# Optimization experiments

Hardware: AMD Instinct MI355X
Metric: run time of the kernel (lower is better)

## Reference

```python
import jax, jax.numpy as jnp
import numpy as np

D_IN = 128      # input_dim == input_edge_dim == output_dim
H = 512         # hidden_dim
D_OUT = 128
O = 100000      # num objects
T = 200000      # num triples/edges


def setup_inputs() -> dict:
    key = jax.random.key(0)
    ks = jax.random.split(key, 12)
    def kaiming(k, fan_in, fan_out):
        # kaiming_normal_ for Linear: std = sqrt(2 / fan_in)
        return jax.random.normal(k, (fan_in, fan_out), jnp.float32) * np.sqrt(2.0 / fan_in)
    obj_vecs = jax.random.normal(ks[0], (O, D_IN), jnp.float32)
    pred_vecs = jax.random.normal(ks[1], (T, D_IN), jnp.float32)
    edges = jax.random.randint(ks[2], (T, 2), 0, O, jnp.int64 if jax.config.jax_enable_x64 else jnp.int32)
    # net1: [3*D_IN -> H -> 2*H + D_OUT], ReLU after each layer
    W1 = kaiming(ks[3], 3 * D_IN, H); b1 = jnp.zeros((H,), jnp.float32)
    W2 = kaiming(ks[4], H, 2 * H + D_OUT); b2 = jnp.zeros((2 * H + D_OUT,), jnp.float32)
    # net2: [H -> H -> D_OUT], ReLU after each layer
    W3 = kaiming(ks[5], H, H); b3 = jnp.zeros((H,), jnp.float32)
    W4 = kaiming(ks[6], H, D_OUT); b4 = jnp.zeros((D_OUT,), jnp.float32)
    return {"obj_vecs": obj_vecs, "pred_vecs": pred_vecs, "edges": edges,
            "W1": W1, "b1": b1, "W2": W2, "b2": b2,
            "W3": W3, "b3": b3, "W4": W4, "b4": b4}


def reference(obj_vecs, pred_vecs, edges, W1, b1, W2, b2, W3, b3, W4, b4):
    s_idx = edges[:, 0]
    o_idx = edges[:, 1]
    # gather + concat: (T, 3*D_IN)
    cur_t = jnp.concatenate([obj_vecs[s_idx], pred_vecs, obj_vecs[o_idx]], axis=1)
    # net1 MLP (final_nonlinearity=True -> ReLU after both layers)
    h = jax.nn.relu(cur_t @ W1 + b1)                 # (T, H)
    new_t = jax.nn.relu(h @ W2 + b2)                 # (T, 2H + D_OUT)
    new_s = new_t[:, :H]
    new_p = new_t[:, H:H + D_OUT]
    new_o = new_t[:, H + D_OUT:]
    # scatter-add pooling over object slots
    n_obj = obj_vecs.shape[0]
    pooled = jnp.zeros((n_obj, H), dtype=obj_vecs.dtype)
    pooled = pooled.at[s_idx].add(new_s).at[o_idx].add(new_o)
    # avg pooling: divide by per-object triple count (clamped at 1)
    ones = jnp.ones((new_s.shape[0],), dtype=obj_vecs.dtype)
    counts = jnp.zeros((n_obj,), dtype=obj_vecs.dtype).at[s_idx].add(ones).at[o_idx].add(ones)
    pooled = pooled / jnp.maximum(counts, 1.0)[:, None]
    # net2 MLP
    new_obj = jax.nn.relu(jax.nn.relu(pooled @ W3 + b3) @ W4 + b4)  # (O, D_OUT)
    return new_obj, new_p
```

## Files before the change

kernel.cpp:

```cpp
#include <hip/hip_runtime.h>
#include <hip/hip_bf16.h>
#include <stdint.h>

typedef __bf16 bf16_t;
typedef __attribute__((ext_vector_type(8))) __bf16 bf16x8;
typedef __attribute__((ext_vector_type(4))) __bf16 bf16x4;
typedef __attribute__((ext_vector_type(4))) float f32x4;

#define O_N 100000
#define T_N 200000
#define LDN 136
#define SCB 98

__device__ __forceinline__ bf16x8 cvt8(const float* p) {
    f32x4 a = *(const f32x4*)p;
    f32x4 b = *(const f32x4*)(p + 4);
    bf16x8 v;
    v[0] = (bf16_t)a[0]; v[1] = (bf16_t)a[1]; v[2] = (bf16_t)a[2]; v[3] = (bf16_t)a[3];
    v[4] = (bf16_t)b[0]; v[5] = (bf16_t)b[1]; v[6] = (bf16_t)b[2]; v[7] = (bf16_t)b[3];
    return v;
}

__device__ __forceinline__ void gload16(const bf16_t* g, bf16_t* l) {
    auto gp = reinterpret_cast<const __attribute__((address_space(1))) void*>(
        reinterpret_cast<uintptr_t>(g));
    auto lp = reinterpret_cast<__attribute__((address_space(3))) void*>(
        reinterpret_cast<uintptr_t>(l));
    __builtin_amdgcn_global_load_lds(gp, lp, 16, 0, 0);
}

__device__ __forceinline__ void swz_block(int& mbase, int& nbase) {
    const int gx   = gridDim.x;
    const int nwg  = gx * gridDim.y;
    const int orig = blockIdx.y * gx + blockIdx.x;
    const int q = nwg >> 3, r = nwg & 7;
    const int xcd = orig & 7, lo = orig >> 3;
    const int base = (xcd < r) ? xcd * (q + 1) : r * (q + 1) + (xcd - r) * q;
    const int id = base + lo;
    nbase = (id % gx) * 128;
    mbase = (id / gx) * 128;
}

template<int MODE, int N, int K>
__launch_bounds__(256)
__global__ void gemm_k(const bf16_t* __restrict__ A,
                       const bf16_t* __restrict__ AobjB,
                       const float*  __restrict__ ApredF,
                       const int*    __restrict__ edges,
                       const float*  __restrict__ countsIn,
                       const bf16_t* __restrict__ Bt,
                       const float*  __restrict__ bias,
                       bf16_t*       __restrict__ CoutB,
                       float*        __restrict__ CoutF,
                       int M)
{
    __shared__ bf16_t smem[32768];
    __shared__ int sIdxL[128], oIdxL[128];

    const int tid  = threadIdx.x;
    const int lane = tid & 63;
    const int wv   = tid >> 6;
    const int wr   = (wv >> 1) * 64;
    const int wc   = (wv & 1) * 64;
    const int fr   = lane & 15;
    const int rowb = tid >> 3;
    const int colS = ((tid & 7) ^ (rowb & 7)) << 3;
    int mbase, nbase;
    swz_block(mbase, nbase);

    if constexpr (MODE == 1) {
        if (tid < 128) {
            int g = mbase + tid; if (g > M - 1) g = M - 1;
            sIdxL[tid] = edges[2 * g];
            oIdxL[tid] = edges[2 * g + 1];
        }
    }
    __syncthreads();

    f32x4 acc[4][4];
    #pragma unroll
    for (int i = 0; i < 4; i++)
        #pragma unroll
        for (int j = 0; j < 4; j++)
            acc[i][j] = (f32x4){0.f, 0.f, 0.f, 0.f};

    auto stage = [&](int p, int k0) {
        bf16_t* lA = smem + p * 16384;
        bf16_t* lB = lA + 8192;
        if constexpr (MODE == 1) {
            if (k0 < 128 || k0 >= 256) {
                const bool sSeg = (k0 < 128);
                const int  seg0 = sSeg ? k0 : (k0 - 256);
                #pragma unroll
                for (int t = 0; t < 4; ++t) {
                    int row = t * 32 + rowb;
                    int gr  = sSeg ? sIdxL[row] : oIdxL[row];
                    gload16(AobjB + (size_t)gr * 128 + seg0 + colS,
                            &lA[t * 2048 + wv * 512]);
                }
            } else {
                #pragma unroll
                for (int t = 0; t < 4; ++t) {
                    int row  = t * 32 + rowb;
                    int grow = mbase + row; if (grow > M - 1) grow = M - 1;
                    bf16x8 v = cvt8(ApredF + (size_t)grow * 128 + (k0 - 128)
                                    + ((tid & 7) << 3));
                    *(bf16x8*)&lA[t * 2048 + rowb * 64 + colS] = v;
                }
            }
        } else {
            #pragma unroll
            for (int t = 0; t < 4; ++t) {
                int row  = t * 32 + rowb;
                int grow = mbase + row; if (grow > M - 1) grow = M - 1;
                gload16(A + (size_t)grow * K + k0 + colS, &lA[t * 2048 + wv * 512]);
            }
        }
        #pragma unroll
        for (int t = 0; t < 4; ++t) {
            int row = t * 32 + rowb;
            gload16(Bt + (size_t)(nbase + row) * K + k0 + colS,
                    &lB[t * 2048 + wv * 512]);
        }
    };

    const int KT = K / 64;
    stage(0, 0);
    asm volatile("s_waitcnt vmcnt(0) lgkmcnt(0)" ::: "memory");
    __builtin_amdgcn_s_barrier();

    int cur = 0;
    for (int kt = 0; kt < KT; ++kt) {
        if (kt + 1 < KT) stage(cur ^ 1, (kt + 1) * 64);
        const bf16_t* lA = smem + cur * 16384;
        const bf16_t* lB = lA + 8192;
        #pragma unroll
        for (int ks8 = 0; ks8 < 8; ks8 += 4) {
            const int c8 = (ks8 + (lane >> 4)) ^ (lane & 7);
            bf16x8 af[4], bfv[4];
            #pragma unroll
            for (int i = 0; i < 4; i++)
                af[i] = *(const bf16x8*)&lA[(wr + i * 16 + fr) * 64 + (c8 << 3)];
            #pragma unroll
            for (int j = 0; j < 4; j++)
                bfv[j] = *(const bf16x8*)&lB[(wc + j * 16 + fr) * 64 + (c8 << 3)];
            #pragma unroll
            for (int i = 0; i < 4; i++)
                #pragma unroll
                for (int j = 0; j < 4; j++) {
                    if constexpr (MODE == 2)
                        acc[i][j] = __builtin_amdgcn_mfma_f32_16x16x32_bf16(
                            bfv[j], af[i], acc[i][j], 0, 0, 0);
                    else
                        acc[i][j] = __builtin_amdgcn_mfma_f32_16x16x32_bf16(
                            af[i], bfv[j], acc[i][j], 0, 0, 0);
                }
        }
        asm volatile("s_waitcnt vmcnt(0) lgkmcnt(0)" ::: "memory");
        __builtin_amdgcn_s_barrier();
        cur ^= 1;
    }

    if constexpr (MODE == 2) {
        const bool isNewp = (nbase == 512);
        const int  cb     = (nbase < 512) ? nbase : (nbase - 128);
        if (isNewp) {
            #pragma unroll
            for (int j = 0; j < 4; j++) {
                int nl = wc + j * 16 + (lane >> 4) * 4;
                f32x4 bv = *(const f32x4*)&bias[nbase + nl];
                #pragma unroll
                for (int i = 0; i < 4; i++) {
                    int ml   = wr + i * 16 + fr;
                    int grow = mbase + ml;
                    if (grow >= M) continue;
                    float v0 = acc[i][j][0] + bv[0]; v0 = v0 > 0.f ? v0 : 0.f;
                    float v1 = acc[i][j][1] + bv[1]; v1 = v1 > 0.f ? v1 : 0.f;
                    float v2 = acc[i][j][2] + bv[2]; v2 = v2 > 0.f ? v2 : 0.f;
                    float v3 = acc[i][j][3] + bv[3]; v3 = v3 > 0.f ? v3 : 0.f;
                    f32x4 o = {v0, v1, v2, v3};
                    *(f32x4*)&CoutF[(size_t)grow * 128 + nl] = o;
                }
            }
        } else {
            #pragma unroll
            for (int j = 0; j < 4; j++) {
                int nl = wc + j * 16 + (lane >> 4) * 4;
                f32x4 bv = *(const f32x4*)&bias[nbase + nl];
                #pragma unroll
                for (int i = 0; i < 4; i++) {
                    int ml = wr + i * 16 + fr;
                    float v0 = acc[i][j][0] + bv[0]; v0 = v0 > 0.f ? v0 : 0.f;
                    float v1 = acc[i][j][1] + bv[1]; v1 = v1 > 0.f ? v1 : 0.f;
                    float v2 = acc[i][j][2] + bv[2]; v2 = v2 > 0.f ? v2 : 0.f;
                    float v3 = acc[i][j][3] + bv[3]; v3 = v3 > 0.f ? v3 : 0.f;
                    bf16x4 pv;
                    pv[0] = (bf16_t)v0; pv[1] = (bf16_t)v1;
                    pv[2] = (bf16_t)v2; pv[3] = (bf16_t)v3;
                    *(bf16x4*)&smem[ml * LDN + nl] = pv;
                }
            }
            __syncthreads();
            #pragma unroll
            for (int rr = 0; rr < 8; ++rr) {
                int row  = rr * 16 + (tid >> 4);
                int grow = mbase + row;
                if (grow >= M) continue;
                bf16x8 v = *(const bf16x8*)&smem[row * LDN + (tid & 15) * 8];
                *(bf16x8*)&CoutB[(size_t)grow * 1024 + cb + (tid & 15) * 8] = v;
            }
        }
    } else {
        float rcv[4][4];
        if constexpr (MODE == 3) {
            #pragma unroll
            for (int i = 0; i < 4; i++)
                #pragma unroll
                for (int r = 0; r < 4; r++) {
                    int grow = mbase + wr + i * 16 + (lane >> 4) * 4 + r;
                    if (grow > M - 1) grow = M - 1;
                    float c = countsIn[grow]; c = c > 1.f ? c : 1.f;
                    rcv[i][r] = 1.f / c;
                }
        }
        #pragma unroll
        for (int j = 0; j < 4; j++) {
            int col = nbase + wc + j * 16 + fr;
            float bval = bias[col];
            #pragma unroll
            for (int i = 0; i < 4; i++) {
                #pragma unroll
                for (int r = 0; r < 4; r++) {
                    int rl   = wr + i * 16 + (lane >> 4) * 4 + r;
                    int grow = mbase + rl;
                    if (grow >= M) continue;
                    float v = acc[i][j][r];
                    if constexpr (MODE == 3) v *= rcv[i][r];
                    v += bval;
                    v = v > 0.f ? v : 0.f;
                    if constexpr (MODE == 4)
                        CoutF[(size_t)grow * N + col] = v;
                    else
                        CoutB[(size_t)grow * N + col] = (bf16_t)v;
                }
            }
        }
    }
}

__global__ void transpose_all_k(const float* __restrict__ W1, bf16_t* __restrict__ W1t,
                                const float* __restrict__ W2, bf16_t* __restrict__ W2t,
                                const float* __restrict__ W3, bf16_t* __restrict__ W3t,
                                const float* __restrict__ W4, bf16_t* __restrict__ W4t) {
    int idx = blockIdx.x * 256 + threadIdx.x;
    const float* in; bf16_t* out; int K, N;
    if (idx < 196608)       { in = W1; out = W1t; K = 384; N = 512;  }
    else if (idx < 786432)  { in = W2; out = W2t; K = 512; N = 1152; idx -= 196608; }
    else if (idx < 1048576) { in = W3; out = W3t; K = 512; N = 512;  idx -= 786432; }
    else if (idx < 1114112) { in = W4; out = W4t; K = 512; N = 128;  idx -= 1048576; }
    else return;
    int k = idx / N, n = idx - k * N;
    out[n * K + k] = (bf16_t)in[idx];
}

__global__ void cvtbf_k(const float* __restrict__ in, bf16_t* __restrict__ out, int n8) {
    int i = blockIdx.x * 256 + threadIdx.x;
    if (i < n8) {
        bf16x8 v = cvt8(in + (size_t)i * 8);
        *(bf16x8*)(out + (size_t)i * 8) = v;
    }
}

__global__ void counts_k(const int* __restrict__ edges, float* __restrict__ counts) {
    int t = blockIdx.x * 256 + threadIdx.x;
    if (t < T_N) {
        unsafeAtomicAdd(&counts[edges[2 * t]],     1.f);
        unsafeAtomicAdd(&counts[edges[2 * t + 1]], 1.f);
    }
}

__launch_bounds__(1024)
__global__ void scan1_k(const float* __restrict__ counts, int* __restrict__ bsum) {
    __shared__ int wsum[16];
    const int tid = threadIdx.x, lane = tid & 63, wv = tid >> 6;
    int i = blockIdx.x * 1024 + tid;
    int v = (i < O_N) ? (int)counts[i] : 0;
    #pragma unroll
    for (int d = 1; d < 64; d <<= 1) v += __shfl_xor(v, d, 64);
    if (lane == 0) wsum[wv] = v;
    __syncthreads();
    if (tid == 0) {
        int s = 0;
        #pragma unroll
        for (int k = 0; k < 16; ++k) s += wsum[k];
        bsum[blockIdx.x] = s;
    }
}
__launch_bounds__(128)
__global__ void scan2_k(const int* __restrict__ bsum, int* __restrict__ bpre,
                        int* __restrict__ offsets) {
    __shared__ int tot0;
    const int tid = threadIdx.x, lane = tid & 63, wv = tid >> 6;
    int x = (tid < SCB) ? bsum[tid] : 0;
    int v = x;
    #pragma unroll
    for (int d = 1; d < 64; d <<= 1) {
        int u = __shfl_up(v, d, 64);
        if (lane >= d) v += u;
    }
    if (tid == 63) tot0 = v;
    __syncthreads();
    if (wv == 1) v += tot0;
    if (tid < SCB) bpre[tid] = v - x;
    if (tid == SCB - 1) offsets[O_N] = v;
}
__launch_bounds__(1024)
__global__ void scan3_k(const float* __restrict__ counts, const int* __restrict__ bpre,
                        int* __restrict__ offsets, int* __restrict__ cursor) {
    __shared__ int wsum[17];
    const int tid = threadIdx.x, lane = tid & 63, wv = tid >> 6;
    int i = blockIdx.x * 1024 + tid;
    int x = (i < O_N) ? (int)counts[i] : 0;
    int v = x;
    #pragma unroll
    for (int d = 1; d < 64; d <<= 1) {
        int u = __shfl_up(v, d, 64);
        if (lane >= d) v += u;
    }
    if (lane == 63) wsum[wv] = v;
    __syncthreads();
    if (tid == 0) {
        int run = bpre[blockIdx.x];
        #pragma unroll
        for (int k = 0; k < 16; ++k) { int t2 = wsum[k]; wsum[k] = run; run += t2; }
    }
    __syncthreads();
    if (i < O_N) { int e = wsum[wv] + (v - x); offsets[i] = e; cursor[i] = e; }
}

__global__ void fill_k(const int* __restrict__ edges, int* __restrict__ cursor,
                       int* __restrict__ slots) {
    int t = blockIdx.x * 256 + threadIdx.x;
    if (t < T_N) {
        int s = edges[2 * t], o = edges[2 * t + 1];
        int p = atomicAdd(&cursor[s], 1);
        slots[p] = t << 1;
        int q = atomicAdd(&cursor[o], 1);
        slots[q] = (t << 1) | 1;
    }
}

template<bool FIRST>
__launch_bounds__(256)
__global__ void pool_k(const bf16_t* __restrict__ newT, const int* __restrict__ offsets,
                       const int* __restrict__ slots, bf16_t* __restrict__ pooledB,
                       int tbase, int tcount) {
    const int gw   = (blockIdx.x * 256 + threadIdx.x) >> 6;
    const int lane = threadIdx.x & 63;
    if (gw >= O_N) return;
    const int s0 = offsets[gw], s1 = offsets[gw + 1];
    float acc[8];
    #pragma unroll
    for (int l = 0; l < 8; l++) acc[l] = 0.f;
    for (int j = s0; j < s1; ++j) {
        int sl = slots[j];
        int lt = (sl >> 1) - tbase;
        if ((unsigned)lt >= (unsigned)tcount) continue;
        const bf16_t* p = newT + (size_t)lt * 1024 + (sl & 1) * 512 + lane * 8;
        bf16x8 v = *(const bf16x8*)p;
        #pragma unroll
        for (int l = 0; l < 8; l++) acc[l] += (float)v[l];
    }
    bf16_t* dst = pooledB + (size_t)gw * 512 + lane * 8;
    if constexpr (!FIRST) {
        bf16x8 prev = *(const bf16x8*)dst;
        #pragma unroll
        for (int l = 0; l < 8; l++) acc[l] += (float)prev[l];
    }
    bf16x8 o;
    #pragma unroll
    for (int l = 0; l < 8; l++) o[l] = (bf16_t)acc[l];
    *(bf16x8*)dst = o;
}

extern "C" void kernel_launch(void* const* d_in, const int* in_sizes, int n_in,
                              void* d_out, int out_size, void* d_ws, size_t ws_size,
                              hipStream_t stream) {
    const float* obj  = (const float*)d_in[0];
    const float* pred = (const float*)d_in[1];
    const int*   edges= (const int*)d_in[2];
    const float* W1 = (const float*)d_in[3];
    const float* b1 = (const float*)d_in[4];
    const float* W2 = (const float*)d_in[5];
    const float* b2 = (const float*)d_in[6];
    const float* W3 = (const float*)d_in[7];
    const float* b3 = (const float*)d_in[8];
    const float* W4 = (const float*)d_in[9];
    const float* b4 = (const float*)d_in[10];
    float* out = (float*)d_out;

    char* ws = (char*)d_ws;
    auto AL = [](size_t x) { return (x + 255) & ~(size_t)255; };

    size_t o_pooled = 0;
    size_t o_counts = AL(o_pooled + (size_t)O_N * 512 * 2);
    size_t o_offs   = AL(o_counts + (size_t)O_N * 4);
    size_t o_curs   = AL(o_offs   + (size_t)(O_N + 1) * 4);
    size_t o_bsum   = AL(o_curs   + (size_t)O_N * 4);
    size_t o_bpre   = AL(o_bsum   + (size_t)128 * 4);
    size_t o_slots  = AL(o_bpre   + (size_t)128 * 4);
    size_t o_objB   = AL(o_slots  + (size_t)2 * T_N * 4);
    size_t o_w1     = AL(o_objB   + (size_t)O_N * 128 * 2);
    size_t o_w2     = AL(o_w1 + (size_t)384 * 512 * 2);
    size_t o_w3     = AL(o_w2 + (size_t)512 * 1152 * 2);
    size_t o_w4     = AL(o_w3 + (size_t)512 * 512 * 2);
    size_t o_chunk  = AL(o_w4 + (size_t)512 * 128 * 2);

    const size_t t3sz = (size_t)O_N * 1024;

    bool fullPool = false;
    int  NCH = 8;
    {
        size_t R2    = (size_t)T_N / 2;
        size_t chunk = AL(R2 * 1024) + (size_t)T_N * 2048;
        size_t need  = o_chunk + (chunk > t3sz ? chunk : t3sz);
        if (ws_size >= need) { fullPool = true; NCH = 2; }
    }
    if (!fullPool) {
        for (int n : {2, 4}) {
            size_t R = (size_t)T_N / n;
            size_t chunk = AL(R * 1024) + R * 2048;
            size_t need  = o_chunk + (chunk > t3sz ? chunk : t3sz);
            if (ws_size >= need) { NCH = n; break; }
        }
    }
    const int R  = T_N / NCH;
    const int MB = (R + 127) / 128;

    bf16_t* pooledB = (bf16_t*)(ws + o_pooled);
    float*  counts  = (float*)(ws + o_counts);
    int*    offs    = (int*)(ws + o_offs);
    int*    curs    = (int*)(ws + o_curs);
    int*    bsum    = (int*)(ws + o_bsum);
    int*    bpre    = (int*)(ws + o_bpre);
    int*    slots   = (int*)(ws + o_slots);
    bf16_t* objB    = (bf16_t*)(ws + o_objB);
    bf16_t* W1t     = (bf16_t*)(ws + o_w1);
    bf16_t* W2t     = (bf16_t*)(ws + o_w2);
    bf16_t* W3t     = (bf16_t*)(ws + o_w3);
    bf16_t* W4t     = (bf16_t*)(ws + o_w4);
    bf16_t* hbuf    = (bf16_t*)(ws + o_chunk);
    bf16_t* newT    = (bf16_t*)(ws + o_chunk + AL((size_t)R * 1024));
    bf16_t* t3      = (bf16_t*)(ws + o_chunk);

    hipMemsetAsync(counts, 0, (size_t)O_N * 4, stream);

    cvtbf_k<<<(O_N * 128 / 8 + 255) / 256, 256, 0, stream>>>(obj, objB, O_N * 128 / 8);
    transpose_all_k<<<(1114112 + 255) / 256, 256, 0, stream>>>(
        W1, W1t, W2, W2t, W3, W3t, W4, W4t);
    counts_k<<<(T_N + 255) / 256, 256, 0, stream>>>(edges, counts);
    scan1_k<<<SCB, 1024, 0, stream>>>(counts, bsum);
    scan2_k<<<1, 128, 0, stream>>>(bsum, bpre, offs);
    scan3_k<<<SCB, 1024, 0, stream>>>(counts, bpre, offs, curs);
    fill_k<<<(T_N + 255) / 256, 256, 0, stream>>>(edges, curs, slots);

    for (int c = 0; c < NCH; ++c) {
        const int row0 = c * R;
        bf16_t* newTc = fullPool ? (newT + (size_t)row0 * 1024) : newT;
        gemm_k<1, 512, 384><<<dim3(4, MB), 256, 0, stream>>>(
            nullptr, objB, pred + (size_t)row0 * 128, edges + 2 * row0,
            nullptr, W1t, b1, hbuf, nullptr, R);
        gemm_k<2, 1152, 512><<<dim3(9, MB), 256, 0, stream>>>(
            hbuf, nullptr, nullptr, nullptr,
            nullptr, W2t, b2, newTc,
            out + (size_t)O_N * 128 + (size_t)row0 * 128, R);
        if (!fullPool) {
            if (c == 0)
                pool_k<true><<<(O_N * 64 + 255) / 256, 256, 0, stream>>>(
                    newT, offs, slots, pooledB, row0, R);
            else
                pool_k<false><<<(O_N * 64 + 255) / 256, 256, 0, stream>>>(
                    newT, offs, slots, pooledB, row0, R);
        }
    }
    if (fullPool)
        pool_k<true><<<(O_N * 64 + 255) / 256, 256, 0, stream>>>(
            newT, offs, slots, pooledB, 0, T_N);

    gemm_k<3, 512, 512><<<dim3(4, 782), 256, 0, stream>>>(
        pooledB, nullptr, nullptr, nullptr, counts,
        W3t, b3, t3, nullptr, O_N);
    gemm_k<4, 128, 512><<<dim3(1, 782), 256, 0, stream>>>(
        t3, nullptr, nullptr, nullptr, nullptr,
        W4t, b4, nullptr, out, O_N);
}
```

Baseline: 1.236 ms.

## Scatter GEMM2 outputs into CSR-sorted slots for contiguous pooling; fuse prep and scans

A new GEMM mode (5) writes each row's new_s and new_o halves directly to its CSR slot position, which fill_k now records per edge. This lets the pooling kernel read contiguous rows instead of gathering them indirectly through the slot list. The prep kernels (bf16 conversion, weight transposes, counts) are merged into one launch, and scan2 is folded into scan3. The old pool_k fallback now loads slot indices once per wave and broadcasts them with shuffles. In exchange, GEMM2 does scattered row writes and the staging buffer grows to 2*T rows.

```diff
diff --git a/kernel.cpp b/kernel.cpp
--- a/kernel.cpp
+++ b/kernel.cpp
@@ -68,7 +68,7 @@
     int mbase, nbase;
     swz_block(mbase, nbase);
 
-    if constexpr (MODE == 1) {
+    if constexpr (MODE == 1 || MODE == 5) {
         if (tid < 128) {
             int g = mbase + tid; if (g > M - 1) g = M - 1;
             sIdxL[tid] = edges[2 * g];
@@ -148,7 +148,7 @@
             for (int i = 0; i < 4; i++)
                 #pragma unroll
                 for (int j = 0; j < 4; j++) {
-                    if constexpr (MODE == 2)
+                    if constexpr (MODE == 2 || MODE == 5)
                         acc[i][j] = __builtin_amdgcn_mfma_f32_16x16x32_bf16(
                             bfv[j], af[i], acc[i][j], 0, 0, 0);
                     else
@@ -161,9 +161,8 @@
         cur ^= 1;
     }
 
-    if constexpr (MODE == 2) {
+    if constexpr (MODE == 2 || MODE == 5) {
         const bool isNewp = (nbase == 512);
-        const int  cb     = (nbase < 512) ? nbase : (nbase - 128);
         if (isNewp) {
             #pragma unroll
             for (int j = 0; j < 4; j++) {
@@ -201,13 +200,21 @@
                 }
             }
             __syncthreads();
+            const bool isS = (nbase < 512);
             #pragma unroll
             for (int rr = 0; rr < 8; ++rr) {
                 int row  = rr * 16 + (tid >> 4);
                 int grow = mbase + row;
                 if (grow >= M) continue;
                 bf16x8 v = *(const bf16x8*)&smem[row * LDN + (tid & 15) * 8];
-                *(bf16x8*)&CoutB[(size_t)grow * 1024 + cb + (tid & 15) * 8] = v;
+                if constexpr (MODE == 2) {
+                    int cb = isS ? nbase : (nbase - 128);
+                    *(bf16x8*)&CoutB[(size_t)grow * 1024 + cb + (tid & 15) * 8] = v;
+                } else {
+                    int cb2  = isS ? nbase : (nbase - 640);
+                    int drow = isS ? sIdxL[row] : oIdxL[row];
+                    *(bf16x8*)&CoutB[(size_t)drow * 512 + cb2 + (tid & 15) * 8] = v;
+                }
             }
         }
     } else {
@@ -248,34 +255,33 @@
     }
 }
 
-__global__ void transpose_all_k(const float* __restrict__ W1, bf16_t* __restrict__ W1t,
-                                const float* __restrict__ W2, bf16_t* __restrict__ W2t,
-                                const float* __restrict__ W3, bf16_t* __restrict__ W3t,
-                                const float* __restrict__ W4, bf16_t* __restrict__ W4t) {
+__global__ void prep_k(const float* __restrict__ obj, bf16_t* __restrict__ objB,
+                       const float* __restrict__ W1, bf16_t* __restrict__ W1t,
+                       const float* __restrict__ W2, bf16_t* __restrict__ W2t,
+                       const float* __restrict__ W3, bf16_t* __restrict__ W3t,
+                       const float* __restrict__ W4, bf16_t* __restrict__ W4t,
+                       const int* __restrict__ edges, float* __restrict__ counts) {
     int idx = blockIdx.x * 256 + threadIdx.x;
-    const float* in; bf16_t* out; int K, N;
-    if (idx < 196608)       { in = W1; out = W1t; K = 384; N = 512;  }
-    else if (idx < 786432)  { in = W2; out = W2t; K = 512; N = 1152; idx -= 196608; }
-    else if (idx < 1048576) { in = W3; out = W3t; K = 512; N = 512;  idx -= 786432; }
-    else if (idx < 1114112) { in = W4; out = W4t; K = 512; N = 128;  idx -= 1048576; }
-    else return;
-    int k = idx / N, n = idx - k * N;
-    out[n * K + k] = (bf16_t)in[idx];
-}
-
-__global__ void cvtbf_k(const float* __restrict__ in, bf16_t* __restrict__ out, int n8) {
-    int i = blockIdx.x * 256 + threadIdx.x;
-    if (i < n8) {
-        bf16x8 v = cvt8(in + (size_t)i * 8);
-        *(bf16x8*)(out + (size_t)i * 8) = v;
-    }
-}
-
-__global__ void counts_k(const int* __restrict__ edges, float* __restrict__ counts) {
-    int t = blockIdx.x * 256 + threadIdx.x;
-    if (t < T_N) {
-        unsafeAtomicAdd(&counts[edges[2 * t]],     1.f);
-        unsafeAtomicAdd(&counts[edges[2 * t + 1]], 1.f);
+    if (idx < 1600000) {
+        bf16x8 v = cvt8(obj + (size_t)idx * 8);
+        *(bf16x8*)(objB + (size_t)idx * 8) = v;
+        return;
+    }
+    idx -= 1600000;
+    if (idx < 1114112) {
+        const float* in; bf16_t* out; int K, N;
+        if (idx < 196608)       { in = W1; out = W1t; K = 384; N = 512;  }
+        else if (idx < 786432)  { in = W2; out = W2t; K = 512; N = 1152; idx -= 196608; }
+        else if (idx < 1048576) { in = W3; out = W3t; K = 512; N = 512;  idx -= 786432; }
+        else                    { in = W4; out = W4t; K = 512; N = 128;  idx -= 1048576; }
+        int k = idx / N, n = idx - k * N;
+        out[n * K + k] = (bf16_t)in[idx];
+        return;
+    }
+    idx -= 1114112;
+    if (idx < T_N) {
+        unsafeAtomicAdd(&counts[edges[2 * idx]],     1.f);
+        unsafeAtomicAdd(&counts[edges[2 * idx + 1]], 1.f);
     }
 }
 
@@ -296,28 +302,12 @@
         bsum[blockIdx.x] = s;
     }
 }
-__launch_bounds__(128)
-__global__ void scan2_k(const int* __restrict__ bsum, int* __restrict__ bpre,
-                        int* __restrict__ offsets) {
-    __shared__ int tot0;
-    const int tid = threadIdx.x, lane = tid & 63, wv = tid >> 6;
-    int x = (tid < SCB) ? bsum[tid] : 0;
-    int v = x;
-    #pragma unroll
-    for (int d = 1; d < 64; d <<= 1) {
-        int u = __shfl_up(v, d, 64);
-        if (lane >= d) v += u;
-    }
-    if (tid == 63) tot0 = v;
-    __syncthreads();
-    if (wv == 1) v += tot0;
-    if (tid < SCB) bpre[tid] = v - x;
-    if (tid == SCB - 1) offsets[O_N] = v;
-}
+
 __launch_bounds__(1024)
-__global__ void scan3_k(const float* __restrict__ counts, const int* __restrict__ bpre,
-                        int* __restrict__ offsets, int* __restrict__ cursor) {
-    __shared__ int wsum[17];
+__global__ void scan23_k(const float* __restrict__ counts, const int* __restrict__ bsum,
+                         int* __restrict__ offsets, int* __restrict__ cursor) {
+    __shared__ int wsum[16];
+    __shared__ int pre2[2];
     const int tid = threadIdx.x, lane = tid & 63, wv = tid >> 6;
     int i = blockIdx.x * 1024 + tid;
     int x = (i < O_N) ? (int)counts[i] : 0;
@@ -328,18 +318,25 @@
         if (lane >= d) v += u;
     }
     if (lane == 63) wsum[wv] = v;
+    if (tid < 128) {
+        int b = (tid < blockIdx.x) ? bsum[tid] : 0;
+        #pragma unroll
+        for (int d = 1; d < 64; d <<= 1) b += __shfl_xor(b, d, 64);
+        if (lane == 0) pre2[tid >> 6] = b;
+    }
     __syncthreads();
     if (tid == 0) {
-        int run = bpre[blockIdx.x];
+        int run = pre2[0] + pre2[1];
         #pragma unroll
         for (int k = 0; k < 16; ++k) { int t2 = wsum[k]; wsum[k] = run; run += t2; }
+        if (blockIdx.x == SCB - 1) offsets[O_N] = run;
     }
     __syncthreads();
     if (i < O_N) { int e = wsum[wv] + (v - x); offsets[i] = e; cursor[i] = e; }
 }
 
 __global__ void fill_k(const int* __restrict__ edges, int* __restrict__ cursor,
-                       int* __restrict__ slots) {
+                       int* __restrict__ slots, int* __restrict__ sslot2) {
     int t = blockIdx.x * 256 + threadIdx.x;
     if (t < T_N) {
         int s = edges[2 * t], o = edges[2 * t + 1];
@@ -347,7 +344,38 @@
         slots[p] = t << 1;
         int q = atomicAdd(&cursor[o], 1);
         slots[q] = (t << 1) | 1;
-    }
+        sslot2[2 * t]     = p;
+        sslot2[2 * t + 1] = q;
+    }
+}
+
+__launch_bounds__(256)
+__global__ void poolS_k(const bf16_t* __restrict__ poolSrc,
+                        const int* __restrict__ offsets,
+                        bf16_t* __restrict__ pooledB) {
+    const int gw   = (blockIdx.x * 256 + threadIdx.x) >> 6;
+    const int lane = threadIdx.x & 63;
+    if (gw >= O_N) return;
+    const int s0 = offsets[gw], s1 = offsets[gw + 1];
+    float acc[8];
+    #pragma unroll
+    for (int l = 0; l < 8; l++) acc[l] = 0.f;
+    int j = s0;
+    for (; j + 1 < s1; j += 2) {
+        bf16x8 a = *(const bf16x8*)(poolSrc + (size_t)j * 512 + lane * 8);
+        bf16x8 b = *(const bf16x8*)(poolSrc + (size_t)(j + 1) * 512 + lane * 8);
+        #pragma unroll
+        for (int l = 0; l < 8; l++) acc[l] += (float)a[l] + (float)b[l];
+    }
+    if (j < s1) {
+        bf16x8 a = *(const bf16x8*)(poolSrc + (size_t)j * 512 + lane * 8);
+        #pragma unroll
+        for (int l = 0; l < 8; l++) acc[l] += (float)a[l];
+    }
+    bf16x8 o;
+    #pragma unroll
+    for (int l = 0; l < 8; l++) o[l] = (bf16_t)acc[l];
+    *(bf16x8*)(pooledB + (size_t)gw * 512 + lane * 8) = o;
 }
 
 template<bool FIRST>
@@ -362,14 +390,18 @@
     float acc[8];
     #pragma unroll
     for (int l = 0; l < 8; l++) acc[l] = 0.f;
-    for (int j = s0; j < s1; ++j) {
-        int sl = slots[j];
-        int lt = (sl >> 1) - tbase;
-        if ((unsigned)lt >= (unsigned)tcount) continue;
-        const bf16_t* p = newT + (size_t)lt * 1024 + (sl & 1) * 512 + lane * 8;
-        bf16x8 v = *(const bf16x8*)p;
-        #pragma unroll
-        for (int l = 0; l < 8; l++) acc[l] += (float)v[l];
+    for (int base = s0; base < s1; base += 64) {
+        int nn = s1 - base; if (nn > 64) nn = 64;
+        int myslot = (lane < nn) ? slots[base + lane] : 0;
+        for (int j = 0; j < nn; ++j) {
+            int sl = __shfl(myslot, j, 64);
+            int lt = (sl >> 1) - tbase;
+            if ((unsigned)lt >= (unsigned)tcount) continue;
+            const bf16_t* p = newT + (size_t)lt * 1024 + (sl & 1) * 512 + lane * 8;
+            bf16x8 v = *(const bf16x8*)p;
+            #pragma unroll
+            for (int l = 0; l < 8; l++) acc[l] += (float)v[l];
+        }
     }
     bf16_t* dst = pooledB + (size_t)gw * 512 + lane * 8;
     if constexpr (!FIRST) {
@@ -407,26 +439,28 @@
     size_t o_offs   = AL(o_counts + (size_t)O_N * 4);
     size_t o_curs   = AL(o_offs   + (size_t)(O_N + 1) * 4);
     size_t o_bsum   = AL(o_curs   + (size_t)O_N * 4);
-    size_t o_bpre   = AL(o_bsum   + (size_t)128 * 4);
-    size_t o_slots  = AL(o_bpre   + (size_t)128 * 4);
-    size_t o_objB   = AL(o_slots  + (size_t)2 * T_N * 4);
+    size_t o_slots  = AL(o_bsum   + (size_t)128 * 4);
+    size_t o_ss2    = AL(o_slots  + (size_t)2 * T_N * 4);
+    size_t o_objB   = AL(o_ss2    + (size_t)2 * T_N * 4);
     size_t o_w1     = AL(o_objB   + (size_t)O_N * 128 * 2);
     size_t o_w2     = AL(o_w1 + (size_t)384 * 512 * 2);
     size_t o_w3     = AL(o_w2 + (size_t)512 * 1152 * 2);
     size_t o_w4     = AL(o_w3 + (size_t)512 * 512 * 2);
     size_t o_chunk  = AL(o_w4 + (size_t)512 * 128 * 2);
 
-    const size_t t3sz = (size_t)O_N * 1024;
-
-    bool fullPool = false;
-    int  NCH = 8;
-    {
-        size_t R2    = (size_t)T_N / 2;
-        size_t chunk = AL(R2 * 1024) + (size_t)T_N * 2048;
+    const size_t t3sz   = (size_t)O_N * 1024;
+    const size_t psSz   = (size_t)2 * T_N * 512 * 2;
+
+    bool scatter = false;
+    int  NCH = 2;
+    for (int n : {2, 4, 8}) {
+        size_t R = (size_t)T_N / n;
+        size_t chunk = AL(R * 1024) + psSz;
         size_t need  = o_chunk + (chunk > t3sz ? chunk : t3sz);
-        if (ws_size >= need) { fullPool = true; NCH = 2; }
-    }
-    if (!fullPool) {
+        if (ws_size >= need) { scatter = true; NCH = n; break; }
+    }
+    if (!scatter) {
+        NCH = 8;
         for (int n : {2, 4}) {
             size_t R = (size_t)T_N / n;
             size_t chunk = AL(R * 1024) + R * 2048;
@@ -442,50 +476,50 @@
     int*    offs    = (int*)(ws + o_offs);
     int*    curs    = (int*)(ws + o_curs);
     int*    bsum    = (int*)(ws + o_bsum);
-    int*    bpre    = (int*)(ws + o_bpre);
     int*    slots   = (int*)(ws + o_slots);
+    int*    sslot2  = (int*)(ws + o_ss2);
     bf16_t* objB    = (bf16_t*)(ws + o_objB);
     bf16_t* W1t     = (bf16_t*)(ws + o_w1);
     bf16_t* W2t     = (bf16_t*)(ws + o_w2);
     bf16_t* W3t     = (bf16_t*)(ws + o_w3);
     bf16_t* W4t     = (bf16_t*)(ws + o_w4);
     bf16_t* hbuf    = (bf16_t*)(ws + o_chunk);
-    bf16_t* newT    = (bf16_t*)(ws + o_chunk + AL((size_t)R * 1024));
+    bf16_t* stage2  = (bf16_t*)(ws + o_chunk + AL((size_t)R * 1024));
     bf16_t* t3      = (bf16_t*)(ws + o_chunk);
 
     hipMemsetAsync(counts, 0, (size_t)O_N * 4, stream);
 
-    cvtbf_k<<<(O_N * 128 / 8 + 255) / 256, 256, 0, stream>>>(obj, objB, O_N * 128 / 8);
-    transpose_all_k<<<(1114112 + 255) / 256, 256, 0, stream>>>(
-        W1, W1t, W2, W2t, W3, W3t, W4, W4t);
-    counts_k<<<(T_N + 255) / 256, 256, 0, stream>>>(edges, counts);
+    prep_k<<<(2914112 + 255) / 256, 256, 0, stream>>>(
+        obj, objB, W1, W1t, W2, W2t, W3, W3t, W4, W4t, edges, counts);
     scan1_k<<<SCB, 1024, 0, stream>>>(counts, bsum);
-    scan2_k<<<1, 128, 0, stream>>>(bsum, bpre, offs);
-    scan3_k<<<SCB, 1024, 0, stream>>>(counts, bpre, offs, curs);
-    fill_k<<<(T_N + 255) / 256, 256, 0, stream>>>(edges, curs, slots);
+    scan23_k<<<SCB, 1024, 0, stream>>>(counts, bsum, offs, curs);
+    fill_k<<<(T_N + 255) / 256, 256, 0, stream>>>(edges, curs, slots, sslot2);
 
     for (int c = 0; c < NCH; ++c) {
         const int row0 = c * R;
-        bf16_t* newTc = fullPool ? (newT + (size_t)row0 * 1024) : newT;
         gemm_k<1, 512, 384><<<dim3(4, MB), 256, 0, stream>>>(
             nullptr, objB, pred + (size_t)row0 * 128, edges + 2 * row0,
             nullptr, W1t, b1, hbuf, nullptr, R);
-        gemm_k<2, 1152, 512><<<dim3(9, MB), 256, 0, stream>>>(
-            hbuf, nullptr, nullptr, nullptr,
-            nullptr, W2t, b2, newTc,
-            out + (size_t)O_N * 128 + (size_t)row0 * 128, R);
-        if (!fullPool) {
+        if (scatter) {
+            gemm_k<5, 1152, 512><<<dim3(9, MB), 256, 0, stream>>>(
+                hbuf, nullptr, nullptr, sslot2 + 2 * row0,
+                nullptr, W2t, b2, stage2,
+                out + (size_t)O_N * 128 + (size_t)row0 * 128, R);
+        } else {
+            gemm_k<2, 1152, 512><<<dim3(9, MB), 256, 0, stream>>>(
+                hbuf, nullptr, nullptr, nullptr,
+                nullptr, W2t, b2, stage2,
+                out + (size_t)O_N * 128 + (size_t)row0 * 128, R);
             if (c == 0)
                 pool_k<true><<<(O_N * 64 + 255) / 256, 256, 0, stream>>>(
-                    newT, offs, slots, pooledB, row0, R);
+                    stage2, offs, slots, pooledB, row0, R);
             else
                 pool_k<false><<<(O_N * 64 + 255) / 256, 256, 0, stream>>>(
-                    newT, offs, slots, pooledB, row0, R);
-        }
-    }
-    if (fullPool)
-        pool_k<true><<<(O_N * 64 + 255) / 256, 256, 0, stream>>>(
-            newT, offs, slots, pooledB, 0, T_N);
+                    stage2, offs, slots, pooledB, row0, R);
+        }
+    }
+    if (scatter)
+        poolS_k<<<(O_N * 64 + 255) / 256, 256, 0, stream>>>(stage2, offs, pooledB);
 
     gemm_k<3, 512, 512><<<dim3(4, 782), 256, 0, stream>>>(
         pooledB, nullptr, nullptr, nullptr, counts,
```

Result: faster. 1.142 ms (-7.6%).
